# Optimization experiments

Hardware: AMD Instinct MI355X
Metric: run time of the kernel (lower is better)

## Reference

```python
import jax, jax.numpy as jnp
import numpy as np

N_NODES = 50000
N_EDGES = 800000
ATOM_F = 64
NBR_F = 64
EPS = 1e-5


def batch_norm(x, gamma, beta):
    # BatchNorm1d in training mode: batch stats, biased variance
    mu = x.mean(axis=0)
    var = x.var(axis=0)
    return gamma * (x - mu) * jax.lax.rsqrt(var + EPS) + beta


def setup_inputs() -> dict:
    key = jax.random.key(0)
    ks = jax.random.split(key, 8)
    d_in = 2 * ATOM_F + NBR_F  # 192
    d_out = 2 * ATOM_F         # 128
    return {
        "atom_in_fea": jax.random.normal(ks[0], (N_NODES, ATOM_F), dtype=jnp.float32),
        "nbr_fea": jax.random.normal(ks[1], (N_EDGES, NBR_F), dtype=jnp.float32),
        "edge_src": jax.random.randint(ks[2], (N_EDGES,), 0, N_NODES),
        "edge_dst": jax.random.randint(ks[3], (N_EDGES,), 0, N_NODES),
        "W_full": jax.random.normal(ks[4], (d_in, d_out), dtype=jnp.float32) / np.sqrt(d_in),
        "b_full": jnp.zeros((d_out,), dtype=jnp.float32),
        "bn1_g": jnp.ones((d_out,), dtype=jnp.float32),
        "bn1_b": jnp.zeros((d_out,), dtype=jnp.float32),
        "bn2_g": jnp.ones((ATOM_F,), dtype=jnp.float32),
        "bn2_b": jnp.zeros((ATOM_F,), dtype=jnp.float32),
    }


def reference(atom_in_fea, nbr_fea, edge_src, edge_dst,
              W_full, b_full, bn1_g, bn1_b, bn2_g, bn2_b):
    # gather endpoint features per edge: [E, 2*A + Nf]
    atom_src = atom_in_fea[edge_src]
    atom_dst = atom_in_fea[edge_dst]
    total = jnp.concatenate([atom_src, atom_dst, nbr_fea], axis=1)
    total = batch_norm(total @ W_full + b_full, bn1_g, bn1_b)  # [E, 2*A]
    filter_fea, core_fea = jnp.split(total, 2, axis=1)
    nbr_msg = jax.nn.sigmoid(filter_fea) * jax.nn.softplus(core_fea)  # [E, A]
    # scatter-add messages back to destination nodes
    atom_update = jax.ops.segment_sum(nbr_msg, edge_dst, num_segments=atom_in_fea.shape[0])
    return jax.nn.softplus(atom_in_fea + batch_norm(atom_update, bn2_g, bn2_b))
```

## Files before the change

kernel.cpp:

```cpp
#include <hip/hip_runtime.h>
#include <hip/hip_fp16.h>
#include <math.h>

#define N_NODES 50000
#define N_EDGES 800000
#define ATOMF 64
#define DIN 192
#define DOUT 128
#define EPB 64
#define NTILES (N_EDGES / EPB)
#define LDW 200
#define NSLOT (EPB * 25)
#define ZLD 136

typedef __attribute__((ext_vector_type(8))) short bf16x8;
typedef __attribute__((ext_vector_type(8))) short s16x8;
typedef __attribute__((ext_vector_type(4))) float f32x4;

__device__ __forceinline__ short f2bf(float f) {
  unsigned u = __float_as_uint(f);
  u += 0x7fffu + ((u >> 16) & 1u);
  return (short)(u >> 16);
}
__device__ __forceinline__ unsigned short f2h(float f) {
  __half h = __float2half_rn(f);
  return *(unsigned short*)&h;
}
__device__ __forceinline__ float h2f(unsigned short u) {
  __half h = *(__half*)&u;
  return __half2float(h);
}
__device__ __forceinline__ float softplus_f(float x) {
  return fmaxf(x, 0.f) + log1pf(__expf(-fabsf(x)));
}
__device__ __forceinline__ float sigmoid_f(float x) {
  return 1.f / (1.f + __expf(-x));
}
__device__ __forceinline__ float fast_sigmoid(float x) {
  return __builtin_amdgcn_rcpf(1.f + __expf(-x));
}
__device__ __forceinline__ float fast_softplus(float x) {
  return fmaxf(x, 0.f) + __logf(1.f + __expf(-fabsf(x)));
}

#define GLOAD16(g, l)                                                          \
  __builtin_amdgcn_global_load_lds(                                            \
      (const __attribute__((address_space(1))) void*)(g),                      \
      (__attribute__((address_space(3))) void*)(l), 16, 0, 0)

__launch_bounds__(256)
__global__ void precvt_k(const float* __restrict__ atom,
                         const float* __restrict__ nbr,
                         const int* __restrict__ edst,
                         unsigned short* __restrict__ atom_bf,
                         unsigned short* __restrict__ nbr_bf,
                         int* __restrict__ deg) {
  const int NA = N_NODES * ATOMF / 8;
  const int NB = N_EDGES * ATOMF / 8;
  int gid = blockIdx.x * blockDim.x + threadIdx.x;
  int stride = gridDim.x * blockDim.x;
  if (deg) {
    for (int i = gid; i < N_EDGES; i += stride) atomicAdd(&deg[edst[i]], 1);
  }
  for (int i = gid; i < NA + NB; i += stride) {
    const float* s;
    unsigned short* d;
    if (i < NA) { s = atom + (size_t)i * 8; d = atom_bf + (size_t)i * 8; }
    else        { s = nbr + (size_t)(i - NA) * 8; d = nbr_bf + (size_t)(i - NA) * 8; }
    float4 a = ((const float4*)s)[0];
    float4 b = ((const float4*)s)[1];
    s16x8 t;
    t[0] = f2bf(a.x); t[1] = f2bf(a.y); t[2] = f2bf(a.z); t[3] = f2bf(a.w);
    t[4] = f2bf(b.x); t[5] = f2bf(b.y); t[6] = f2bf(b.z); t[7] = f2bf(b.w);
    *(s16x8*)d = t;
  }
}

__launch_bounds__(1024)
__global__ void scan_k(const int* __restrict__ deg,
                       int* __restrict__ rowptr,
                       int* __restrict__ cursor) {
  __shared__ int wsum[16];
  const int tid = threadIdx.x;
  const int lane = tid & 63, wv = tid >> 6;
  const int N4 = N_NODES / 4;
  int base = 0;
  for (int c0 = 0; c0 < N4; c0 += 1024) {
    int i4 = c0 + tid;
    int4 v = make_int4(0, 0, 0, 0);
    if (i4 < N4) v = ((const int4*)deg)[i4];
    int t = v.x + v.y + v.z + v.w;
    int s = t;
    #pragma unroll
    for (int d = 1; d < 64; d <<= 1) {
      int u = __shfl_up(s, d, 64);
      if (lane >= d) s += u;
    }
    if (lane == 63) wsum[wv] = s;
    __syncthreads();
    if (wv == 0 && lane < 16) {
      int ws = wsum[lane];
      #pragma unroll
      for (int d = 1; d < 16; d <<= 1) {
        int u = __shfl_up(ws, d, 64);
        if (lane >= d) ws += u;
      }
      wsum[lane] = ws;
    }
    __syncthreads();
    int wbase = wv ? wsum[wv - 1] : 0;
    int excl = base + wbase + s - t;
    if (i4 < N4) {
      int4 r;
      r.x = excl;
      r.y = excl + v.x;
      r.z = r.y + v.y;
      r.w = r.z + v.z;
      ((int4*)rowptr)[i4] = r;
      ((int4*)cursor)[i4] = r;
    }
    int tot = wsum[15];
    __syncthreads();
    base += tot;
  }
  if (tid == 0) rowptr[N_NODES] = base;
}

__launch_bounds__(256)
__global__ void fill_k(const int* __restrict__ edst,
                       int* __restrict__ cursor,
                       int* __restrict__ iperm) {
  int gid = blockIdx.x * 256 + threadIdx.x;
  if (gid < N_EDGES) {
    int pos = atomicAdd(&cursor[edst[gid]], 1);
    iperm[gid] = pos;
  }
}

__device__ __forceinline__ void stage_tile(const unsigned short* __restrict__ atom_bf,
                                           const unsigned short* __restrict__ nbr_bf,
                                           const int* __restrict__ esrc,
                                           const int* __restrict__ edst,
                                           int e0, unsigned short* lbase,
                                           const int* g_enc, int wv) {
  #pragma unroll
  for (int it = 0; it < 7; ++it) {
    if (it * 256 + wv * 64 < NSLOT) {
      int e = g_enc[it];
      int row = e & 255;
      int coff = (e >> 8) & 255;
      int sel = e >> 16;
      const unsigned short* src;
      if (sel < 2) {
        const int* ip = sel ? edst : esrc;
        int idx = ip[e0 + row];
        src = atom_bf + (size_t)idx * ATOMF + coff;
      } else {
        src = nbr_bf + (size_t)(e0 + row) * ATOMF + coff;
      }
      GLOAD16(src, lbase + (size_t)(it * 256 + wv * 64) * 8);
    }
  }
}

__launch_bounds__(256, 4)
__global__ void edge_gemm(const unsigned short* __restrict__ atom_bf,
                          const unsigned short* __restrict__ nbr_bf,
                          const int* __restrict__ esrc,
                          const int* __restrict__ edst,
                          const int* __restrict__ iperm,
                          const float* __restrict__ W,
                          float* __restrict__ stats,
                          unsigned short* __restrict__ zc) {
  __shared__ unsigned short Tl[EPB * LDW];

  const int tid = threadIdx.x;
  const int lane = tid & 63;
  const int wv = tid >> 6;
  const int l15 = lane & 15;
  const int lg = lane >> 4;
  const int colF = wv * 16 + l15;
  const int colC = colF + 64;

  bf16x8 wf[2][6];
  #pragma unroll
  for (int cg = 0; cg < 2; ++cg) {
    #pragma unroll
    for (int kk = 0; kk < 6; ++kk) {
      bf16x8 t;
      #pragma unroll
      for (int jj = 0; jj < 8; ++jj)
        t[jj] = f2bf(W[(size_t)(kk * 32 + lg * 8 + jj) * 128 + cg * 64 + colF]);
      wf[cg][kk] = t;
    }
  }

  int g_enc[7];
  #pragma unroll
  for (int it = 0; it < 7; ++it) {
    int s = it * 256 + tid;
    if (s >= NSLOT) s = 0;
    int row = s / 25;
    int w = s - row * 25;
    int sel, coff;
    if (w < 8)       { sel = 0; coff = w * 8; }
    else if (w < 16) { sel = 1; coff = (w - 8) * 8; }
    else             { sel = 2; coff = (w < 24 ? (w - 16) * 8 : 0); }
    g_enc[it] = row | (coff << 8) | (sel << 16);
  }

  const int orow = tid >> 2;
  const int oq = tid & 3;

  float fs[2] = {0.f, 0.f}, fq[2] = {0.f, 0.f};

  for (int tile = blockIdx.x; tile < NTILES; tile += gridDim.x) {
    stage_tile(atom_bf, nbr_bf, esrc, edst, tile * EPB, Tl, g_enc, wv);
    __syncthreads();

    f32x4 acc[2][4] = {};
    #pragma unroll
    for (int rg = 0; rg < 4; ++rg) {
      #pragma unroll
      for (int kk = 0; kk < 6; ++kk) {
        bf16x8 a = *(const bf16x8*)&Tl[(rg * 16 + l15) * LDW + kk * 32 + lg * 8];
        acc[0][rg] = __builtin_amdgcn_mfma_f32_16x16x32_bf16(a, wf[0][kk], acc[0][rg], 0, 0, 0);
        acc[1][rg] = __builtin_amdgcn_mfma_f32_16x16x32_bf16(a, wf[1][kk], acc[1][rg], 0, 0, 0);
      }
    }

    #pragma unroll
    for (int cg = 0; cg < 2; ++cg) {
      #pragma unroll
      for (int rg = 0; rg < 4; ++rg) {
        float z0 = acc[cg][rg][0], z1 = acc[cg][rg][1];
        float z2 = acc[cg][rg][2], z3 = acc[cg][rg][3];
        fs[cg] += (z0 + z1) + (z2 + z3);
        fq[cg] += z0 * z0 + z1 * z1 + z2 * z2 + z3 * z3;
      }
    }

    __syncthreads();

    #pragma unroll
    for (int cg = 0; cg < 2; ++cg)
      #pragma unroll
      for (int rg = 0; rg < 4; ++rg)
        #pragma unroll
        for (int r = 0; r < 4; ++r)
          Tl[(rg * 16 + lg * 4 + r) * ZLD + cg * 64 + colF] = f2h(acc[cg][rg][r]);

    __syncthreads();

    {
      int pos = iperm[tile * 64 + orow];
      const s16x8* src = (const s16x8*)&Tl[orow * ZLD + oq * 32];
      s16x8 v0 = src[0], v1 = src[1], v2 = src[2], v3 = src[3];
      unsigned short* dst = zc + (size_t)pos * 128 + oq * 32;
      *(s16x8*)dst = v0;
      *(s16x8*)(dst + 8) = v1;
      *(s16x8*)(dst + 16) = v2;
      *(s16x8*)(dst + 24) = v3;
    }

    __syncthreads();
  }

  #pragma unroll
  for (int cg = 0; cg < 2; ++cg) {
    fs[cg] += __shfl_xor(fs[cg], 16, 64); fs[cg] += __shfl_xor(fs[cg], 32, 64);
    fq[cg] += __shfl_xor(fq[cg], 16, 64); fq[cg] += __shfl_xor(fq[cg], 32, 64);
  }
  if (lane < 16) {
    atomicAdd(&stats[colF], fs[0]);
    atomicAdd(&stats[colC], fs[1]);
    atomicAdd(&stats[128 + colF], fq[0]);
    atomicAdd(&stats[128 + colC], fq[1]);
  }
}

__global__ void finalize1_k(const float* __restrict__ stats,
                            const float* __restrict__ g,
                            const float* __restrict__ be,
                            float* __restrict__ ab) {
  int n = threadIdx.x;
  float mu = stats[n] * (1.f / N_EDGES);
  float var = stats[128 + n] * (1.f / N_EDGES) - mu * mu;
  float a = g[n] * rsqrtf(var + 1e-5f);
  ab[n] = a;
  ab[128 + n] = be[n] - mu * a;
}

__launch_bounds__(256)
__global__ void gather_k(const unsigned short* __restrict__ zc,
                         const int* __restrict__ rowptr,
                         const float* __restrict__ ab,
                         float* __restrict__ out) {
  int n = blockIdx.x * 4 + (threadIdx.x >> 6);
  if (n >= N_NODES) return;
  int c = threadIdx.x & 63;
  float af = ab[c], cf = ab[128 + c];
  float ag = ab[64 + c], cg2 = ab[192 + c];
  int s = rowptr[n], e = rowptr[n + 1];
  float acc = 0.f;
  for (int i = s; i < e; ++i) {
    const unsigned short* row = zc + (size_t)i * 128;
    float f = af * h2f(row[c]) + cf;
    float g = ag * h2f(row[64 + c]) + cg2;
    acc += fast_sigmoid(f) * fast_softplus(g);
  }
  out[(size_t)n * 64 + c] = acc;
}

__launch_bounds__(256)
__global__ void stats2_k(const float* __restrict__ upd, float* __restrict__ stats2) {
  int tid = threadIdx.x;
  int gid = blockIdx.x * 256 + tid;
  int stride = gridDim.x * 256;
  float4 s = make_float4(0.f, 0.f, 0.f, 0.f);
  float4 q = make_float4(0.f, 0.f, 0.f, 0.f);
  for (int i = gid; i < N_NODES * 16; i += stride) {
    float4 v = ((const float4*)upd)[i];
    s.x += v.x; s.y += v.y; s.z += v.z; s.w += v.w;
    q.x += v.x * v.x; q.y += v.y * v.y; q.z += v.z * v.z; q.w += v.w * v.w;
  }
  int lane = tid & 63;
  int wv = tid >> 6;
  s.x += __shfl_xor(s.x, 16, 64); s.x += __shfl_xor(s.x, 32, 64);
  s.y += __shfl_xor(s.y, 16, 64); s.y += __shfl_xor(s.y, 32, 64);
  s.z += __shfl_xor(s.z, 16, 64); s.z += __shfl_xor(s.z, 32, 64);
  s.w += __shfl_xor(s.w, 16, 64); s.w += __shfl_xor(s.w, 32, 64);
  q.x += __shfl_xor(q.x, 16, 64); q.x += __shfl_xor(q.x, 32, 64);
  q.y += __shfl_xor(q.y, 16, 64); q.y += __shfl_xor(q.y, 32, 64);
  q.z += __shfl_xor(q.z, 16, 64); q.z += __shfl_xor(q.z, 32, 64);
  q.w += __shfl_xor(q.w, 16, 64); q.w += __shfl_xor(q.w, 32, 64);
  __shared__ float red[4 * 128];
  if (lane < 16) {
    int f = lane * 4;
    red[wv * 128 + f + 0] = s.x; red[wv * 128 + f + 1] = s.y;
    red[wv * 128 + f + 2] = s.z; red[wv * 128 + f + 3] = s.w;
    red[wv * 128 + 64 + f + 0] = q.x; red[wv * 128 + 64 + f + 1] = q.y;
    red[wv * 128 + 64 + f + 2] = q.z; red[wv * 128 + 64 + f + 3] = q.w;
  }
  __syncthreads();
  if (tid < 128) {
    float v = red[tid] + red[128 + tid] + red[256 + tid] + red[384 + tid];
    atomicAdd(&stats2[tid], v);
  }
}

__global__ void finalize2_k(const float* __restrict__ stats2,
                            const float* __restrict__ g,
                            const float* __restrict__ be,
                            float* __restrict__ ab2) {
  int f = threadIdx.x;
  float mu = stats2[f] * (1.f / N_NODES);
  float var = stats2[64 + f] * (1.f / N_NODES) - mu * mu;
  float a = g[f] * rsqrtf(var + 1e-5f);
  ab2[f] = a;
  ab2[64 + f] = be[f] - mu * a;
}

__launch_bounds__(256)
__global__ void out_k(const float* __restrict__ atom,
                      const float* __restrict__ ab2,
                      float* __restrict__ out) {
  int gid = blockIdx.x * 256 + threadIdx.x;
  int stride = gridDim.x * 256;
  for (int i = gid; i < N_NODES * 16; i += stride) {
    float4 u = ((const float4*)out)[i];
    float4 x = ((const float4*)atom)[i];
    int f = (i & 15) * 4;
    float4 r;
    r.x = softplus_f(x.x + u.x * ab2[f + 0] + ab2[64 + f + 0]);
    r.y = softplus_f(x.y + u.y * ab2[f + 1] + ab2[64 + f + 1]);
    r.z = softplus_f(x.z + u.z * ab2[f + 2] + ab2[64 + f + 2]);
    r.w = softplus_f(x.w + u.w * ab2[f + 3] + ab2[64 + f + 3]);
    ((float4*)out)[i] = r;
  }
}

template<int PASS>
__launch_bounds__(256, 2)
__global__ void edge_pass(const float* __restrict__ atom,
                          const float* __restrict__ nbr,
                          const int* __restrict__ esrc,
                          const int* __restrict__ edst,
                          const float* __restrict__ W,
                          const float* __restrict__ bvec,
                          float* __restrict__ stats,
                          const float* __restrict__ ab,
                          float* __restrict__ upd) {
  __shared__ short Wl[DOUT * LDW];
  __shared__ short Tl[EPB * LDW];
  __shared__ int eix[2 * EPB];

  const int tid = threadIdx.x;
  const int lane = tid & 63;
  const int wv = tid >> 6;
  const int l15 = lane & 15;
  const int lg = lane >> 4;

  for (int i = tid; i < DIN * DOUT; i += 256) {
    int k = i >> 7, n = i & 127;
    Wl[n * LDW + k] = f2bf(W[i]);
  }
  float bcol[8], acol[8], ccol[8];
  #pragma unroll
  for (int j = 0; j < 8; ++j) {
    int n = j * 16 + l15;
    bcol[j] = bvec[n];
    if constexpr (PASS == 1) { acol[j] = ab[n]; ccol[j] = ab[DOUT + n]; }
    else { acol[j] = 0.f; ccol[j] = 0.f; }
  }
  float fsum[8], fsq[8];
  #pragma unroll
  for (int j = 0; j < 8; ++j) { fsum[j] = 0.f; fsq[j] = 0.f; }

  for (int tile = blockIdx.x; tile < NTILES; tile += gridDim.x) {
    const int e0 = tile * EPB;
    __syncthreads();
    if (tid < EPB) eix[tid] = esrc[e0 + tid];
    else if (tid < 2 * EPB) eix[tid] = edst[e0 + tid - EPB];
    __syncthreads();
    for (int i = tid; i < EPB * 96; i += 256) {
      int row = i / 96;
      int cl = (i - row * 96) * 2;
      const float* p;
      if (cl < 64)       p = atom + (size_t)eix[row] * 64 + cl;
      else if (cl < 128) p = atom + (size_t)eix[EPB + row] * 64 + (cl - 64);
      else               p = nbr + (size_t)(e0 + row) * 64 + (cl - 128);
      float2 v = *(const float2*)p;
      unsigned pk = (unsigned)(unsigned short)f2bf(v.x)
                  | ((unsigned)(unsigned short)f2bf(v.y) << 16);
      *(unsigned*)&Tl[row * LDW + cl] = pk;
    }
    __syncthreads();
    f32x4 acc[8] = {};
    const int abase = (wv * 16 + l15) * LDW + lg * 8;
    #pragma unroll
    for (int kk = 0; kk < 6; ++kk) {
      bf16x8 afr = *(const bf16x8*)&Tl[abase + kk * 32];
      #pragma unroll
      for (int j = 0; j < 8; ++j) {
        bf16x8 bfr = *(const bf16x8*)&Wl[(j * 16 + l15) * LDW + lg * 8 + kk * 32];
        acc[j] = __builtin_amdgcn_mfma_f32_16x16x32_bf16(afr, bfr, acc[j], 0, 0, 0);
      }
    }
    if constexpr (PASS == 0) {
      #pragma unroll
      for (int j = 0; j < 8; ++j)
        #pragma unroll
        for (int r = 0; r < 4; ++r) {
          float z = acc[j][r] + bcol[j];
          fsum[j] += z; fsq[j] += z * z;
        }
    } else {
      #pragma unroll
      for (int r = 0; r < 4; ++r) {
        int row = wv * 16 + lg * 4 + r;
        int d = eix[EPB + row];
        float* urow = upd + (size_t)d * 64;
        #pragma unroll
        for (int j = 0; j < 4; ++j) {
          float f = (acc[j][r] + bcol[j]) * acol[j] + ccol[j];
          float g = (acc[j + 4][r] + bcol[j + 4]) * acol[j + 4] + ccol[j + 4];
          atomicAdd(&urow[j * 16 + l15], sigmoid_f(f) * softplus_f(g));
        }
      }
    }
  }
  if constexpr (PASS == 0) {
    #pragma unroll
    for (int j = 0; j < 8; ++j) {
      fsum[j] += __shfl_xor(fsum[j], 16, 64);
      fsum[j] += __shfl_xor(fsum[j], 32, 64);
      fsq[j]  += __shfl_xor(fsq[j], 16, 64);
      fsq[j]  += __shfl_xor(fsq[j], 32, 64);
    }
    __syncthreads();
    float* redf = (float*)Tl;
    if (lane < 16) {
      #pragma unroll
      for (int j = 0; j < 8; ++j) {
        redf[wv * 256 + j * 16 + lane] = fsum[j];
        redf[wv * 256 + 128 + j * 16 + lane] = fsq[j];
      }
    }
    __syncthreads();
    float s = redf[tid] + redf[256 + tid] + redf[512 + tid] + redf[768 + tid];
    atomicAdd(&stats[tid], s);
  }
}

extern "C" void kernel_launch(void* const* d_in, const int* in_sizes, int n_in,
                              void* d_out, int out_size, void* d_ws, size_t ws_size,
                              hipStream_t stream) {
  const float* atom = (const float*)d_in[0];
  const float* nbr  = (const float*)d_in[1];
  const int*   esrc = (const int*)d_in[2];
  const int*   edst = (const int*)d_in[3];
  const float* W    = (const float*)d_in[4];
  const float* bvec = (const float*)d_in[5];
  const float* g1   = (const float*)d_in[6];
  const float* b1   = (const float*)d_in[7];
  const float* g2   = (const float*)d_in[8];
  const float* b2   = (const float*)d_in[9];
  float* out = (float*)d_out;
  char* ws = (char*)d_ws;

  float* stats1 = (float*)ws;
  float* ab1    = stats1 + 256;
  float* stats2 = stats1 + 512;
  float* ab2    = stats1 + 640;

  const size_t OFF_ATOM = 4096;
  const size_t SZ_ATOM  = (size_t)N_NODES * ATOMF * 2;
  const size_t OFF_NBR  = OFF_ATOM + SZ_ATOM;
  const size_t SZ_NBR   = (size_t)N_EDGES * ATOMF * 2;
  const size_t OFF_ZT   = OFF_NBR + SZ_NBR;
  const size_t SZ_ZT    = (size_t)N_EDGES * DOUT * 2;
  const size_t OFF_PERM = OFF_ZT + SZ_ZT;
  const size_t SZ_PERM  = (size_t)N_EDGES * 4;
  const size_t OFF_DEG  = OFF_PERM + SZ_PERM;
  const size_t OFF_RP   = OFF_DEG + N_NODES * 4;
  const size_t OFF_CUR  = OFF_RP + (N_NODES + 1) * 4 + 12;
  const size_t NEED_NEW = OFF_CUR + N_NODES * 4;

  hipMemsetAsync(stats1, 0, 768 * sizeof(float), stream);

  if (ws_size >= NEED_NEW) {
    unsigned short* atom_bf = (unsigned short*)(ws + OFF_ATOM);
    unsigned short* nbr_bf  = (unsigned short*)(ws + OFF_NBR);
    unsigned short* zc      = (unsigned short*)(ws + OFF_ZT);
    int* iperm  = (int*)(ws + OFF_PERM);
    int* deg    = (int*)(ws + OFF_DEG);
    int* rowptr = (int*)(ws + OFF_RP);
    int* cursor = (int*)(ws + OFF_CUR);

    hipMemsetAsync(deg, 0, N_NODES * sizeof(int), stream);
    precvt_k<<<2048, 256, 0, stream>>>(atom, nbr, edst, atom_bf, nbr_bf, deg);
    scan_k<<<1, 1024, 0, stream>>>(deg, rowptr, cursor);
    fill_k<<<(N_EDGES + 255) / 256, 256, 0, stream>>>(edst, cursor, iperm);

    edge_gemm<<<1024, 256, 0, stream>>>(atom_bf, nbr_bf, esrc, edst, iperm,
                                        W, stats1, zc);
    finalize1_k<<<1, 128, 0, stream>>>(stats1, g1, b1, ab1);

    gather_k<<<(N_NODES + 3) / 4, 256, 0, stream>>>(zc, rowptr, ab1, out);
  } else {
    hipMemsetAsync(out, 0, (size_t)N_NODES * 64 * sizeof(float), stream);
    edge_pass<0><<<512, 256, 0, stream>>>(atom, nbr, esrc, edst, W, bvec,
                                          stats1, nullptr, nullptr);
    finalize1_k<<<1, 128, 0, stream>>>(stats1, g1, b1, ab1);
    edge_pass<1><<<512, 256, 0, stream>>>(atom, nbr, esrc, edst, W, bvec,
                                          nullptr, ab1, out);
  }

  stats2_k<<<512, 256, 0, stream>>>(out, stats2);
  finalize2_k<<<1, 64, 0, stream>>>(stats2, g2, b2, ab2);
  out_k<<<512, 256, 0, stream>>>(atom, ab2, out);
}
```

Before: 452.9 us.

## Load gathered GEMM operands directly into registers instead of staging via LDS

The edge GEMM no longer stages the gathered source, destination and neighbour rows into shared memory with global_load_lds. Each lane now loads its bf16x8 MFMA A-fragments straight from global memory using the edge indices, which removes one barrier per tile and shrinks LDS to the output staging buffer. The gather kernel's inner loop is also unrolled by two to raise memory-level parallelism. In exchange, the direct register loads are less coalesced and sit on the MFMA critical path with no explicit prefetch.

```diff
diff --git a/kernel.cpp b/kernel.cpp
--- a/kernel.cpp
+++ b/kernel.cpp
@@ -10,7 +10,6 @@
 #define EPB 64
 #define NTILES (N_EDGES / EPB)
 #define LDW 200
-#define NSLOT (EPB * 25)
 #define ZLD 136
 
 typedef __attribute__((ext_vector_type(8))) short bf16x8;
@@ -42,11 +41,6 @@
 __device__ __forceinline__ float fast_softplus(float x) {
   return fmaxf(x, 0.f) + __logf(1.f + __expf(-fabsf(x)));
 }
-
-#define GLOAD16(g, l)                                                          \
-  __builtin_amdgcn_global_load_lds(                                            \
-      (const __attribute__((address_space(1))) void*)(g),                      \
-      (__attribute__((address_space(3))) void*)(l), 16, 0, 0)
 
 __launch_bounds__(256)
 __global__ void precvt_k(const float* __restrict__ atom,
@@ -137,32 +131,6 @@
   }
 }
 
-__device__ __forceinline__ void stage_tile(const unsigned short* __restrict__ atom_bf,
-                                           const unsigned short* __restrict__ nbr_bf,
-                                           const int* __restrict__ esrc,
-                                           const int* __restrict__ edst,
-                                           int e0, unsigned short* lbase,
-                                           const int* g_enc, int wv) {
-  #pragma unroll
-  for (int it = 0; it < 7; ++it) {
-    if (it * 256 + wv * 64 < NSLOT) {
-      int e = g_enc[it];
-      int row = e & 255;
-      int coff = (e >> 8) & 255;
-      int sel = e >> 16;
-      const unsigned short* src;
-      if (sel < 2) {
-        const int* ip = sel ? edst : esrc;
-        int idx = ip[e0 + row];
-        src = atom_bf + (size_t)idx * ATOMF + coff;
-      } else {
-        src = nbr_bf + (size_t)(e0 + row) * ATOMF + coff;
-      }
-      GLOAD16(src, lbase + (size_t)(it * 256 + wv * 64) * 8);
-    }
-  }
-}
-
 __launch_bounds__(256, 4)
 __global__ void edge_gemm(const unsigned short* __restrict__ atom_bf,
                           const unsigned short* __restrict__ nbr_bf,
@@ -172,7 +140,7 @@
                           const float* __restrict__ W,
                           float* __restrict__ stats,
                           unsigned short* __restrict__ zc) {
-  __shared__ unsigned short Tl[EPB * LDW];
+  __shared__ unsigned short Zl[EPB * ZLD];
 
   const int tid = threadIdx.x;
   const int lane = tid & 63;
@@ -195,38 +163,39 @@
     }
   }
 
-  int g_enc[7];
-  #pragma unroll
-  for (int it = 0; it < 7; ++it) {
-    int s = it * 256 + tid;
-    if (s >= NSLOT) s = 0;
-    int row = s / 25;
-    int w = s - row * 25;
-    int sel, coff;
-    if (w < 8)       { sel = 0; coff = w * 8; }
-    else if (w < 16) { sel = 1; coff = (w - 8) * 8; }
-    else             { sel = 2; coff = (w < 24 ? (w - 16) * 8 : 0); }
-    g_enc[it] = row | (coff << 8) | (sel << 16);
-  }
-
   const int orow = tid >> 2;
   const int oq = tid & 3;
 
   float fs[2] = {0.f, 0.f}, fq[2] = {0.f, 0.f};
 
   for (int tile = blockIdx.x; tile < NTILES; tile += gridDim.x) {
-    stage_tile(atom_bf, nbr_bf, esrc, edst, tile * EPB, Tl, g_enc, wv);
-    __syncthreads();
+    const int e0 = tile * EPB;
 
     f32x4 acc[2][4] = {};
     #pragma unroll
     for (int rg = 0; rg < 4; ++rg) {
-      #pragma unroll
-      for (int kk = 0; kk < 6; ++kk) {
-        bf16x8 a = *(const bf16x8*)&Tl[(rg * 16 + l15) * LDW + kk * 32 + lg * 8];
-        acc[0][rg] = __builtin_amdgcn_mfma_f32_16x16x32_bf16(a, wf[0][kk], acc[0][rg], 0, 0, 0);
-        acc[1][rg] = __builtin_amdgcn_mfma_f32_16x16x32_bf16(a, wf[1][kk], acc[1][rg], 0, 0, 0);
-      }
+      int e = e0 + rg * 16 + l15;
+      const unsigned short* srcb = atom_bf + (size_t)esrc[e] * ATOMF + lg * 8;
+      const unsigned short* dstb = atom_bf + (size_t)edst[e] * ATOMF + lg * 8;
+      const unsigned short* nbrb = nbr_bf + (size_t)e * ATOMF + lg * 8;
+      bf16x8 a0 = *(const bf16x8*)srcb;
+      bf16x8 a1 = *(const bf16x8*)(srcb + 32);
+      bf16x8 a2 = *(const bf16x8*)dstb;
+      bf16x8 a3 = *(const bf16x8*)(dstb + 32);
+      bf16x8 a4 = *(const bf16x8*)nbrb;
+      bf16x8 a5 = *(const bf16x8*)(nbrb + 32);
+      acc[0][rg] = __builtin_amdgcn_mfma_f32_16x16x32_bf16(a0, wf[0][0], acc[0][rg], 0, 0, 0);
+      acc[1][rg] = __builtin_amdgcn_mfma_f32_16x16x32_bf16(a0, wf[1][0], acc[1][rg], 0, 0, 0);
+      acc[0][rg] = __builtin_amdgcn_mfma_f32_16x16x32_bf16(a1, wf[0][1], acc[0][rg], 0, 0, 0);
+      acc[1][rg] = __builtin_amdgcn_mfma_f32_16x16x32_bf16(a1, wf[1][1], acc[1][rg], 0, 0, 0);
+      acc[0][rg] = __builtin_amdgcn_mfma_f32_16x16x32_bf16(a2, wf[0][2], acc[0][rg], 0, 0, 0);
+      acc[1][rg] = __builtin_amdgcn_mfma_f32_16x16x32_bf16(a2, wf[1][2], acc[1][rg], 0, 0, 0);
+      acc[0][rg] = __builtin_amdgcn_mfma_f32_16x16x32_bf16(a3, wf[0][3], acc[0][rg], 0, 0, 0);
+      acc[1][rg] = __builtin_amdgcn_mfma_f32_16x16x32_bf16(a3, wf[1][3], acc[1][rg], 0, 0, 0);
+      acc[0][rg] = __builtin_amdgcn_mfma_f32_16x16x32_bf16(a4, wf[0][4], acc[0][rg], 0, 0, 0);
+      acc[1][rg] = __builtin_amdgcn_mfma_f32_16x16x32_bf16(a4, wf[1][4], acc[1][rg], 0, 0, 0);
+      acc[0][rg] = __builtin_amdgcn_mfma_f32_16x16x32_bf16(a5, wf[0][5], acc[0][rg], 0, 0, 0);
+      acc[1][rg] = __builtin_amdgcn_mfma_f32_16x16x32_bf16(a5, wf[1][5], acc[1][rg], 0, 0, 0);
     }
 
     #pragma unroll
@@ -248,13 +217,13 @@
       for (int rg = 0; rg < 4; ++rg)
         #pragma unroll
         for (int r = 0; r < 4; ++r)
-          Tl[(rg * 16 + lg * 4 + r) * ZLD + cg * 64 + colF] = f2h(acc[cg][rg][r]);
+          Zl[(rg * 16 + lg * 4 + r) * ZLD + cg * 64 + colF] = f2h(acc[cg][rg][r]);
 
     __syncthreads();
 
     {
       int pos = iperm[tile * 64 + orow];
-      const s16x8* src = (const s16x8*)&Tl[orow * ZLD + oq * 32];
+      const s16x8* src = (const s16x8*)&Zl[orow * ZLD + oq * 32];
       s16x8 v0 = src[0], v1 = src[1], v2 = src[2], v3 = src[3];
       unsigned short* dst = zc + (size_t)pos * 128 + oq * 32;
       *(s16x8*)dst = v0;
@@ -262,8 +231,6 @@
       *(s16x8*)(dst + 16) = v2;
       *(s16x8*)(dst + 24) = v3;
     }
-
-    __syncthreads();
   }
 
   #pragma unroll
@@ -303,11 +270,22 @@
   float ag = ab[64 + c], cg2 = ab[192 + c];
   int s = rowptr[n], e = rowptr[n + 1];
   float acc = 0.f;
-  for (int i = s; i < e; ++i) {
-    const unsigned short* row = zc + (size_t)i * 128;
-    float f = af * h2f(row[c]) + cf;
-    float g = ag * h2f(row[64 + c]) + cg2;
-    acc += fast_sigmoid(f) * fast_softplus(g);
+  int i = s;
+  for (; i + 2 <= e; i += 2) {
+    const unsigned short* r0 = zc + (size_t)i * 128;
+    const unsigned short* r1 = r0 + 128;
+    float f0 = af * h2f(r0[c]) + cf;
+    float g0 = ag * h2f(r0[64 + c]) + cg2;
+    float f1 = af * h2f(r1[c]) + cf;
+    float g1 = ag * h2f(r1[64 + c]) + cg2;
+    acc += fast_sigmoid(f0) * fast_softplus(g0);
+    acc += fast_sigmoid(f1) * fast_softplus(g1);
+  }
+  if (i < e) {
+    const unsigned short* r0 = zc + (size_t)i * 128;
+    float f0 = af * h2f(r0[c]) + cf;
+    float g0 = ag * h2f(r0[64 + c]) + cg2;
+    acc += fast_sigmoid(f0) * fast_softplus(g0);
   }
   out[(size_t)n * 64 + c] = acc;
 }
```

Result: faster. 443.9 us (-2.0%).
